# Performance work log

Measured on AMD Instinct MI355X. Metric: run time of the kernel, lower is better.

## Reference

```python
import jax, jax.numpy as jnp
import numpy as np

BETA = 9.0
BETA2 = BETA * BETA / 2.0  # 40.5
D = 256
N1 = 8192
N2 = 8192
ALPHA = 30.0


def setup_inputs() -> dict:
    key = jax.random.key(0)
    k1, k2, k3, k4 = jax.random.split(key, 4)
    pointset1 = jax.random.uniform(k1, (N1, 3), dtype=jnp.float32)
    pointset2 = jax.random.uniform(k2, (N2, 3), dtype=jnp.float32)
    # A ~ (approx) strict standard normal columns, scaled by alpha
    A = jax.random.normal(k3, (3, D), dtype=jnp.float32) * ALPHA
    P = jax.random.normal(k4, (3, D), dtype=jnp.float32)
    return {"pointset1": pointset1, "pointset2": pointset2, "A": A, "P": P}


def reference(pointset1, pointset2, A, P):
    d = A.shape[1]
    sqrt_d = jnp.asarray(d, jnp.float32) ** 0.5
    # complex random Fourier features exp(i x @ A)
    eP1 = jnp.exp(1j * (pointset1 @ A))  # (n, d) complex64
    eP2 = jnp.exp(1j * (pointset2 @ A))  # (N, d) complex64
    # pairwise squared distances without (n, N, 3) intermediate
    sq1 = jnp.sum(pointset1 * pointset1, axis=-1, keepdims=True)      # (n, 1)
    sq2 = jnp.sum(pointset2 * pointset2, axis=-1, keepdims=True).T    # (1, N)
    D2 = sq1 + sq2 - 2.0 * (pointset1 @ pointset2.T)                  # (n, N)
    J = jnp.exp(-BETA2 * D2)                                          # Gaussian kernel adjacency
    # weighted aggregation of complex features, done on real/imag parts
    G = (J @ jnp.real(eP2)) + 1j * (J @ jnp.imag(eP2))                # (n, d)
    G = G / eP1
    G = G / jnp.linalg.norm(G, axis=-1, keepdims=True) * sqrt_d
    G = G + jnp.exp(1j * (pointset1 @ P))  # positional encoding
    # return real-valued view: (n, d, 2) = [real, imag]
    return jnp.stack([jnp.real(G), jnp.imag(G)], axis=-1)
```

## Files before the change

kernel.cpp:

```cpp
#include <hip/hip_runtime.h>
#include <math.h>

#define N1 8192
#define N2 8192
#define KS 4096
#define B2L  58.42914916f
#define B2L2 116.85829832f

typedef short bf16x8 __attribute__((ext_vector_type(8)));
typedef float f32x4 __attribute__((ext_vector_type(4)));
typedef unsigned short ushort8 __attribute__((ext_vector_type(8)));

#define LBAR() do { \
    asm volatile("s_waitcnt lgkmcnt(0)" ::: "memory"); \
    __builtin_amdgcn_s_barrier(); \
} while (0)

__device__ __forceinline__ unsigned short bf16bits(float f) {
    union { float f; unsigned u; } x; x.f = f;
    unsigned r = x.u + 0x7fff + ((x.u >> 16) & 1);
    return (unsigned short)(r >> 16);
}

__device__ __forceinline__ unsigned int cvt_pk_bf16(float a, float b) {
    unsigned int r;
    asm("v_cvt_pk_bf16_f32 %0, %1, %2" : "=v"(r) : "v"(a), "v"(b));
    return r;
}

__device__ __forceinline__ float fast_exp2(float x) {
    float r;
    asm("v_exp_f32 %0, %1" : "=v"(r) : "v"(x));
    return r;
}

__global__ __launch_bounds__(512) void feat_kernel(const float* __restrict__ p2,
                                                   const float* __restrict__ A,
                                                   unsigned short* __restrict__ Vf) {
    __shared__ float p2s[24];
    const int t = threadIdx.x;
    const int j0 = blockIdx.x * 8;
    if (t < 24) p2s[t] = p2[(size_t)j0 * 3 + t];
    __syncthreads();
    const int k = t & 255, part = t >> 8;
    const float a0 = A[k], a1 = A[256 + k], a2 = A[512 + k];
    ushort8 v8;
    #pragma unroll
    for (int j = 0; j < 8; ++j) {
        float th = fmaf(p2s[j * 3], a0, fmaf(p2s[j * 3 + 1], a1, p2s[j * 3 + 2] * a2));
        float s, c;
        sincosf(th, &s, &c);
        v8[j] = bf16bits(part ? s : c);
    }
    *(ushort8*)(Vf + (size_t)blockIdx.x * 4096 + t * 8) = v8;
}

__device__ __forceinline__ void loadQ(const float* __restrict__ p2, int kbase, int qoff,
                                      float& qx0, float& qy0, float& qz0, float& e20,
                                      float& qx1, float& qy1, float& qz1, float& e21) {
    const float* q = p2 + (size_t)(unsigned)(kbase * 3) + qoff;
    qx0 = q[0]; qy0 = q[1]; qz0 = q[2];
    qx1 = q[3]; qy1 = q[4]; qz1 = q[5];
    e20 = -B2L * fmaf(qx0, qx0, fmaf(qy0, qy0, qz0 * qz0));
    e21 = -B2L * fmaf(qx1, qx1, fmaf(qy1, qy1, qz1 * qz1));
}

__device__ __forceinline__ void buildJ(unsigned int* __restrict__ Jdst, const int wrOfs[4],
                                       const float px[4], const float py[4],
                                       const float pz[4], const float e1[4],
                                       float qx0, float qy0, float qz0, float e20,
                                       float qx1, float qy1, float qz1, float e21) {
    #pragma unroll
    for (int rr = 0; rr < 4; ++rr) {
        float s0 = fmaf(px[rr], qx0, fmaf(py[rr], qy0, pz[rr] * qz0));
        float s1 = fmaf(px[rr], qx1, fmaf(py[rr], qy1, pz[rr] * qz1));
        float j0 = fast_exp2(fmaf(s0, B2L2, e1[rr] + e20));
        float j1 = fast_exp2(fmaf(s1, B2L2, e1[rr] + e21));
        *(unsigned int*)((char*)Jdst + wrOfs[rr]) = cvt_pk_bf16(j0, j1);
    }
}

__device__ __forceinline__ void loadB(bf16x8 b[2][2], const unsigned short* __restrict__ pB,
                                      const int bOfs[2][2]) {
    #pragma unroll
    for (int kk = 0; kk < 2; ++kk)
        #pragma unroll
        for (int nr = 0; nr < 2; ++nr)
            b[kk][nr] = *(const bf16x8*)(pB + bOfs[kk][nr]);
}

__device__ __forceinline__ void mfmaStep(f32x4 acc[4][2], const unsigned int* __restrict__ Jsrc,
                                         bf16x8 b[2][2], const int rdOfs[2][4]) {
    #pragma unroll
    for (int kk = 0; kk < 2; ++kk)
        #pragma unroll
        for (int mr = 0; mr < 4; ++mr) {
            bf16x8 af = *(const bf16x8*)((const char*)Jsrc + rdOfs[kk][mr]);
            acc[mr][0] = __builtin_amdgcn_mfma_f32_16x16x32_bf16(af, b[kk][0], acc[mr][0], 0, 0, 0);
            acc[mr][1] = __builtin_amdgcn_mfma_f32_16x16x32_bf16(af, b[kk][1], acc[mr][1], 0, 0, 0);
        }
}

__global__ __launch_bounds__(512, 4) void gemm_kernel(const float* __restrict__ p1,
                                                      const float* __restrict__ p2,
                                                      const unsigned short* __restrict__ Vf,
                                                      float* __restrict__ pout0,
                                                      float* __restrict__ pout1) {
    __shared__ unsigned int JA[2048];
    __shared__ unsigned int JB[2048];

    const int t = threadIdx.x;
    const int l = t & 63;
    const int w = t >> 6;
    const int g = l >> 4;
    const int ln = l & 15;
    const int bid = (int)blockIdx.x;
    const int ks = (bid & 7) >> 2;
    const int cg = bid & 1;
    const int rb = (bid >> 3) * 2 + ((bid >> 1) & 1);
    const int i0 = rb * 64;
    const int k0 = ks * KS;

    const int kp = t & 31;
    const int tm = t >> 5;
    const int qoff = kp * 6;
    float px[4], py[4], pz[4], e1[4];
    int wrOfs[4];
    #pragma unroll
    for (int rr = 0; rr < 4; ++rr) {
        const float* pp = p1 + (size_t)(i0 + tm + rr * 16) * 3;
        px[rr] = pp[0]; py[rr] = pp[1]; pz[rr] = pp[2];
        e1[rr] = -B2L * fmaf(px[rr], px[rr], fmaf(py[rr], py[rr], pz[rr] * pz[rr]));
        int m = tm + rr * 16;
        wrOfs[rr] = (m * 128 + kp * 4) ^ ((m & 7) << 4);
    }

    int rdOfs[2][4];
    #pragma unroll
    for (int kk = 0; kk < 2; ++kk)
        #pragma unroll
        for (int mr = 0; mr < 4; ++mr) {
            int m = mr * 16 + ln;
            rdOfs[kk][mr] = (m * 128 + kk * 64 + g * 16) ^ ((m & 7) << 4);
        }

    int bOfs[2][2];
    #pragma unroll
    for (int kk = 0; kk < 2; ++kk)
        #pragma unroll
        for (int nr = 0; nr < 2; ++nr)
            bOfs[kk][nr] = (kk * 4 + g) * 4096 + (cg * 256 + w * 32 + nr * 16 + ln) * 8;

    f32x4 acc[4][2] = {};

    bf16x8 bA_[2][2], bB_[2][2];
    float qx0, qy0, qz0, e20, qx1, qy1, qz1, e21;
    float rx0, ry0, rz0, f20, rx1, ry1, rz1, f21;

    loadQ(p2, k0, qoff, qx0, qy0, qz0, e20, qx1, qy1, qz1, e21);
    buildJ(JA, wrOfs, px, py, pz, e1, qx0, qy0, qz0, e20, qx1, qy1, qz1, e21);
    loadB(bA_, Vf + ((unsigned)k0 >> 3) * 4096u, bOfs);
    loadQ(p2, k0 + 64, qoff, rx0, ry0, rz0, f20, rx1, ry1, rz1, f21);

    for (int jc = k0; jc < k0 + KS; jc += 128) {
        LBAR();
        loadB(bB_, Vf + ((unsigned)((jc + 64) & (N2 - 1)) >> 3) * 4096u, bOfs);
        buildJ(JB, wrOfs, px, py, pz, e1, rx0, ry0, rz0, f20, rx1, ry1, rz1, f21);
        loadQ(p2, (jc + 128) & (N2 - 1), qoff, qx0, qy0, qz0, e20, qx1, qy1, qz1, e21);
        mfmaStep(acc, JA, bA_, rdOfs);
        LBAR();
        loadB(bA_, Vf + ((unsigned)((jc + 128) & (N2 - 1)) >> 3) * 4096u, bOfs);
        buildJ(JA, wrOfs, px, py, pz, e1, qx0, qy0, qz0, e20, qx1, qy1, qz1, e21);
        loadQ(p2, (jc + 192) & (N2 - 1), qoff, rx0, ry0, rz0, f20, rx1, ry1, rz1, f21);
        mfmaStep(acc, JB, bB_, rdOfs);
    }

    float* outb = ks ? pout1 : pout0;
    #pragma unroll
    for (int mr = 0; mr < 4; ++mr) {
        #pragma unroll
        for (int reg = 0; reg < 4; ++reg) {
            int row = i0 + mr * 16 + g * 4 + reg;
            #pragma unroll
            for (int nr = 0; nr < 2; ++nr) {
                int kc = w * 32 + nr * 16 + ln;
                outb[((size_t)row * 256 + kc) * 2 + cg] = acc[mr][nr][reg];
            }
        }
    }
}

__global__ __launch_bounds__(256) void epi_kernel(const float* __restrict__ p1,
                                                  const float* __restrict__ A,
                                                  const float* __restrict__ P,
                                                  const float* __restrict__ part0,
                                                  float* __restrict__ out) {
    __shared__ float wsum[4];
    const int i = blockIdx.x;
    const int k = threadIdx.x;
    const size_t idx = ((size_t)i * 256 + k) * 2;
    float2 g0 = *(const float2*)(part0 + idx);
    float2 g1 = *(const float2*)(out + idx);
    const float gr = g0.x + g1.x;
    const float gi = g0.y + g1.y;

    float sq = fmaf(gr, gr, gi * gi);
    #pragma unroll
    for (int off = 1; off < 64; off <<= 1) sq += __shfl_xor(sq, off, 64);
    if ((k & 63) == 0) wsum[k >> 6] = sq;
    __syncthreads();
    const float ns = wsum[0] + wsum[1] + wsum[2] + wsum[3];
    const float scale = 16.0f * rsqrtf(ns);

    const float x = p1[(size_t)i * 3 + 0], y = p1[(size_t)i * 3 + 1], z = p1[(size_t)i * 3 + 2];
    float th1 = fmaf(x, A[k], fmaf(y, A[256 + k], z * A[512 + k]));
    float thp = fmaf(x, P[k], fmaf(y, P[256 + k], z * P[512 + k]));
    float s1, c1, sp, cp;
    sincosf(th1, &s1, &c1);
    sincosf(thp, &sp, &cp);
    float2 res;
    res.x = fmaf(gr, c1, gi * s1) * scale + cp;
    res.y = fmaf(gi, c1, -gr * s1) * scale + sp;
    *(float2*)(out + idx) = res;
}

extern "C" void kernel_launch(void* const* d_in, const int* in_sizes, int n_in,
                              void* d_out, int out_size, void* d_ws, size_t ws_size,
                              hipStream_t stream) {
    const float* p1 = (const float*)d_in[0];
    const float* p2 = (const float*)d_in[1];
    const float* A  = (const float*)d_in[2];
    const float* P  = (const float*)d_in[3];
    unsigned short* Vf = (unsigned short*)d_ws;
    float* part0 = (float*)((char*)d_ws + (size_t)8388608);
    float* out = (float*)d_out;

    feat_kernel<<<N2 / 8, 512, 0, stream>>>(p2, A, Vf);
    gemm_kernel<<<512, 512, 0, stream>>>(p1, p2, Vf, part0, out);
    epi_kernel<<<N1, 256, 0, stream>>>(p1, A, P, part0, out);
}
```

Before: 127.7 us.

## Stage B feature tiles into LDS via async global_load_lds double buffering

Replaces per-wave direct global register loads of the bf16 feature matrix with asynchronous global-to-LDS copies into two double-buffered LDS tiles, which all waves of the block then read. Barriers now also wait on vmcnt so the staged data is complete before use. The block index mapping is changed so column-group and K-split pairs are adjacent. This adds 64KB of LDS per block, which may limit occupancy, and the full vmcnt wait at each barrier also stalls on the outstanding point loads.

```diff
diff --git a/kernel.cpp b/kernel.cpp
--- a/kernel.cpp
+++ b/kernel.cpp
@@ -11,8 +11,8 @@
 typedef float f32x4 __attribute__((ext_vector_type(4)));
 typedef unsigned short ushort8 __attribute__((ext_vector_type(8)));
 
-#define LBAR() do { \
-    asm volatile("s_waitcnt lgkmcnt(0)" ::: "memory"); \
+#define FBAR() do { \
+    asm volatile("s_waitcnt vmcnt(0) lgkmcnt(0)" ::: "memory"); \
     __builtin_amdgcn_s_barrier(); \
 } while (0)
 
@@ -80,25 +80,37 @@
     }
 }
 
-__device__ __forceinline__ void loadB(bf16x8 b[2][2], const unsigned short* __restrict__ pB,
-                                      const int bOfs[2][2]) {
-    #pragma unroll
-    for (int kk = 0; kk < 2; ++kk)
-        #pragma unroll
-        for (int nr = 0; nr < 2; ++nr)
-            b[kk][nr] = *(const bf16x8*)(pB + bOfs[kk][nr]);
+__device__ __forceinline__ void stageB(const unsigned short* __restrict__ Vf,
+                                       unsigned short* lds, int kbIdx8, int cgOff,
+                                       int wv, int l) {
+    const char* g0 = (const char*)Vf + (size_t)(unsigned)kbIdx8 * 8192u + (unsigned)cgOff
+                     + (unsigned)(wv & 3) * 1024u + (unsigned)l * 16u;
+    char* l0 = (char*)lds + (unsigned)(wv & 3) * 1024u;
+    const int kbBase = wv >> 2;
+    #pragma unroll
+    for (int i = 0; i < 4; ++i) {
+        int kb = 2 * i + kbBase;
+        __builtin_amdgcn_global_load_lds(
+            (const __attribute__((address_space(1))) unsigned int*)(g0 + (unsigned)kb * 8192u),
+            (__attribute__((address_space(3))) unsigned int*)(l0 + (unsigned)kb * 4096u),
+            16, 0, 0);
+    }
 }
 
 __device__ __forceinline__ void mfmaStep(f32x4 acc[4][2], const unsigned int* __restrict__ Jsrc,
-                                         bf16x8 b[2][2], const int rdOfs[2][4]) {
-    #pragma unroll
-    for (int kk = 0; kk < 2; ++kk)
+                                         const unsigned short* __restrict__ Bl,
+                                         const int rdOfs[2][4], const int lbOfs[2][2]) {
+    #pragma unroll
+    for (int kk = 0; kk < 2; ++kk) {
+        bf16x8 b0 = *(const bf16x8*)((const char*)Bl + lbOfs[kk][0]);
+        bf16x8 b1 = *(const bf16x8*)((const char*)Bl + lbOfs[kk][1]);
         #pragma unroll
         for (int mr = 0; mr < 4; ++mr) {
             bf16x8 af = *(const bf16x8*)((const char*)Jsrc + rdOfs[kk][mr]);
-            acc[mr][0] = __builtin_amdgcn_mfma_f32_16x16x32_bf16(af, b[kk][0], acc[mr][0], 0, 0, 0);
-            acc[mr][1] = __builtin_amdgcn_mfma_f32_16x16x32_bf16(af, b[kk][1], acc[mr][1], 0, 0, 0);
+            acc[mr][0] = __builtin_amdgcn_mfma_f32_16x16x32_bf16(af, b0, acc[mr][0], 0, 0, 0);
+            acc[mr][1] = __builtin_amdgcn_mfma_f32_16x16x32_bf16(af, b1, acc[mr][1], 0, 0, 0);
         }
+    }
 }
 
 __global__ __launch_bounds__(512, 4) void gemm_kernel(const float* __restrict__ p1,
@@ -108,6 +120,8 @@
                                                       float* __restrict__ pout1) {
     __shared__ unsigned int JA[2048];
     __shared__ unsigned int JB[2048];
+    __shared__ __align__(16) unsigned short Blds0[16384];
+    __shared__ __align__(16) unsigned short Blds1[16384];
 
     const int t = threadIdx.x;
     const int l = t & 63;
@@ -115,11 +129,11 @@
     const int g = l >> 4;
     const int ln = l & 15;
     const int bid = (int)blockIdx.x;
-    const int ks = (bid & 7) >> 2;
     const int cg = bid & 1;
-    const int rb = (bid >> 3) * 2 + ((bid >> 1) & 1);
-    const int i0 = rb * 64;
+    const int ks = (bid >> 1) & 1;
+    const int i0 = (bid >> 2) * 64;
     const int k0 = ks * KS;
+    const int cgOff = cg * 4096;
 
     const int kp = t & 31;
     const int tm = t >> 5;
@@ -144,35 +158,34 @@
             rdOfs[kk][mr] = (m * 128 + kk * 64 + g * 16) ^ ((m & 7) << 4);
         }
 
-    int bOfs[2][2];
+    int lbOfs[2][2];
     #pragma unroll
     for (int kk = 0; kk < 2; ++kk)
         #pragma unroll
         for (int nr = 0; nr < 2; ++nr)
-            bOfs[kk][nr] = (kk * 4 + g) * 4096 + (cg * 256 + w * 32 + nr * 16 + ln) * 8;
+            lbOfs[kk][nr] = (kk * 4 + g) * 4096 + (w * 32 + nr * 16 + ln) * 16;
 
     f32x4 acc[4][2] = {};
 
-    bf16x8 bA_[2][2], bB_[2][2];
     float qx0, qy0, qz0, e20, qx1, qy1, qz1, e21;
     float rx0, ry0, rz0, f20, rx1, ry1, rz1, f21;
 
+    stageB(Vf, Blds0, k0 >> 3, cgOff, w, l);
     loadQ(p2, k0, qoff, qx0, qy0, qz0, e20, qx1, qy1, qz1, e21);
     buildJ(JA, wrOfs, px, py, pz, e1, qx0, qy0, qz0, e20, qx1, qy1, qz1, e21);
-    loadB(bA_, Vf + ((unsigned)k0 >> 3) * 4096u, bOfs);
     loadQ(p2, k0 + 64, qoff, rx0, ry0, rz0, f20, rx1, ry1, rz1, f21);
 
     for (int jc = k0; jc < k0 + KS; jc += 128) {
-        LBAR();
-        loadB(bB_, Vf + ((unsigned)((jc + 64) & (N2 - 1)) >> 3) * 4096u, bOfs);
+        FBAR();
+        stageB(Vf, Blds1, ((jc + 64) & (N2 - 1)) >> 3, cgOff, w, l);
         buildJ(JB, wrOfs, px, py, pz, e1, rx0, ry0, rz0, f20, rx1, ry1, rz1, f21);
         loadQ(p2, (jc + 128) & (N2 - 1), qoff, qx0, qy0, qz0, e20, qx1, qy1, qz1, e21);
-        mfmaStep(acc, JA, bA_, rdOfs);
-        LBAR();
-        loadB(bA_, Vf + ((unsigned)((jc + 128) & (N2 - 1)) >> 3) * 4096u, bOfs);
+        mfmaStep(acc, JA, Blds0, rdOfs, lbOfs);
+        FBAR();
+        stageB(Vf, Blds0, ((jc + 128) & (N2 - 1)) >> 3, cgOff, w, l);
         buildJ(JA, wrOfs, px, py, pz, e1, qx0, qy0, qz0, e20, qx1, qy1, qz1, e21);
         loadQ(p2, (jc + 192) & (N2 - 1), qoff, rx0, ry0, rz0, f20, rx1, ry1, rz1, f21);
-        mfmaStep(acc, JB, bB_, rdOfs);
+        mfmaStep(acc, JB, Blds1, rdOfs, lbOfs);
     }
 
     float* outb = ks ? pout1 : pout0;
```

Result: no change. 127.5 us (-0.2%).
